# Optimization experiments

Measured on AMD Instinct MI355X. Metric: run time of the kernel, lower is better.

## Reference

```python
import jax, jax.numpy as jnp
import numpy as np

B, N, D, H, T = 2048, 128, 256, 8, 64
HD = D // H
TANH_C = 10.0
MASK_PENALTY = 1e9


def setup_inputs() -> dict:
    key = jax.random.key(0)
    ks = jax.random.split(key, 16)
    s = 1.0 / np.sqrt(D).astype(np.float32)
    w = lambda k: jax.random.normal(k, (D, D), jnp.float32) * s
    return {
        'node_emb': jax.random.normal(ks[0], (B, N, D), jnp.float32),
        'graph_emb': jax.random.normal(ks[1], (B, D), jnp.float32),
        'W_target': w(ks[2]), 'W_global': w(ks[3]),
        'W_K1': w(ks[4]), 'W_K2': w(ks[5]),
        'W_Q': w(ks[6]), 'W_V': w(ks[7]),
        'Wq_m': w(ks[8]), 'Wk_m': w(ks[9]), 'Wv_m': w(ks[10]), 'Wo_m': w(ks[11]),
        'targets': jax.random.randint(ks[12], (T, B), 0, N, jnp.int32),
        'masks': jax.random.randint(ks[13], (T, B, N), 0, 2, jnp.int32),
    }


def _mha(q, k, v, Wq, Wk, Wv, Wo):
    # q: [B,1,D]; k,v: [B,N,D]. Standard multi-head attention (glimpse).
    qh = (q @ Wq.T).reshape(B, 1, H, HD).transpose(0, 2, 1, 3)   # [B,H,1,HD]
    kh = (k @ Wk.T).reshape(B, N, H, HD).transpose(0, 2, 1, 3)   # [B,H,N,HD]
    vh = (v @ Wv.T).reshape(B, N, H, HD).transpose(0, 2, 1, 3)
    scores = jnp.einsum('bhqd,bhnd->bhqn', qh, kh) / np.sqrt(HD).astype(np.float32)
    attn = jax.nn.softmax(scores, axis=-1)
    out = jnp.einsum('bhqn,bhnd->bhqd', attn, vh)                # [B,H,1,HD]
    out = out.transpose(0, 2, 1, 3).reshape(B, 1, D)
    return out @ Wo.T


def reference(node_emb, graph_emb, W_target, W_global, W_K1, W_K2, W_Q, W_V,
              Wq_m, Wk_m, Wv_m, Wo_m, targets, masks):
    # Step-invariant projections (embeddings fixed across decode steps here).
    keys = node_emb @ W_K1.T      # [B,N,D]
    vals = node_emb @ W_V.T       # [B,N,D]
    key2 = node_emb @ W_K2.T      # [B,N,D]
    g_ctx = graph_emb @ W_global.T  # [B,D]
    inv_sqrt_d = np.float32(1.0 / np.sqrt(D))

    def step(ll, tm):
        tgt, mask = tm  # tgt:[B] int32, mask:[B,N] int32
        tgt_emb = jnp.take_along_axis(node_emb, tgt[:, None, None], axis=1)[:, 0, :]  # [B,D]
        context = (tgt_emb @ W_target.T + g_ctx)[:, None, :]      # [B,1,D]
        glimpse = _mha(context, keys, vals, Wq_m, Wk_m, Wv_m, Wo_m)  # [B,1,D]
        query = glimpse @ W_Q.T                                    # [B,1,D]
        logits = jnp.einsum('bqd,bnd->bn', query, key2) * inv_sqrt_d  # [B,N]
        logits = TANH_C * jnp.tanh(logits) - mask.astype(jnp.float32) * MASK_PENALTY
        log_p = jax.nn.log_softmax(logits, axis=1)
        actions = jnp.argmax(log_p, axis=1)                        # greedy TopKSampler
        ll = ll + jnp.take_along_axis(log_p, actions[:, None], axis=1)[:, 0]
        return ll, None

    ll, _ = jax.lax.scan(step, jnp.zeros(B, jnp.float32), (targets, masks))
    return ll
```

## Files before the change

kernel.cpp:

```cpp
#include <hip/hip_runtime.h>
#include <hip/hip_bf16.h>

#define BB 2048
#define NN 128
#define DD 256
#define HH 8
#define TT 64

typedef __bf16 bf16x8 __attribute__((ext_vector_type(8)));
typedef float f32x4 __attribute__((ext_vector_type(4)));

static __device__ __forceinline__ f32x4 mfma16(bf16x8 a, bf16x8 b, f32x4 c) {
  return __builtin_amdgcn_mfma_f32_16x16x32_bf16(a, b, c, 0, 0, 0);
}

static __device__ __forceinline__ f32x4 zero4() {
  f32x4 z = {0.f, 0.f, 0.f, 0.f};
  return z;
}

static __device__ __forceinline__ bf16x8 cvt8(const float* p) {
  const float4 x0 = *(const float4*)p;
  const float4 x1 = *(const float4*)(p + 4);
  bf16x8 r;
  r[0] = (__bf16)x0.x; r[1] = (__bf16)x0.y; r[2] = (__bf16)x0.z; r[3] = (__bf16)x0.w;
  r[4] = (__bf16)x1.x; r[5] = (__bf16)x1.y; r[6] = (__bf16)x1.z; r[7] = (__bf16)x1.w;
  return r;
}

static __device__ __forceinline__ unsigned pk2(float a, float b) {
  __bf16 x = (__bf16)a, y = (__bf16)b;
  unsigned short ux, uy;
  __builtin_memcpy(&ux, &x, 2);
  __builtin_memcpy(&uy, &y, 2);
  return (unsigned)ux | ((unsigned)uy << 16);
}

static __device__ __forceinline__ float fast_tanh10(float y) {
  const float e = __expf(2.f * y);
  return 10.f - 20.f * __builtin_amdgcn_rcpf(1.f + e);
}

__global__ void fold1(const float* __restrict__ Wq_m, const float* __restrict__ W_target,
                      const float* __restrict__ W_global, const float* __restrict__ Wk_m,
                      const float* __restrict__ W_K1, const float* __restrict__ Wv_m,
                      const float* __restrict__ W_V, const float* __restrict__ W_Q,
                      const float* __restrict__ Wo_m,
                      __bf16* __restrict__ WTQ, float* __restrict__ WGQT,
                      __bf16* __restrict__ WKH, __bf16* __restrict__ WVH,
                      float* __restrict__ WQO) {
  const int p = blockIdx.x >> 8;
  const int i = blockIdx.x & 255;
  const int t = threadIdx.x;
  __shared__ float arow[256];
  const float* A;
  const float* Bm;
  if (p == 0)      { A = Wq_m; Bm = W_target; }
  else if (p == 1) { A = Wq_m; Bm = W_global; }
  else if (p == 2) { A = Wk_m; Bm = W_K1; }
  else if (p == 3) { A = Wv_m; Bm = W_V; }
  else             { A = W_Q;  Bm = Wo_m; }
  arow[t] = A[i * 256 + t];
  __syncthreads();
  float acc = 0.f;
  for (int k = 0; k < 256; ++k) acc = fmaf(arow[k], Bm[k * 256 + t], acc);
  if (p == 0)      WTQ[i * 256 + t] = (__bf16)acc;
  else if (p == 1) WGQT[t * 256 + i] = acc;
  else if (p == 2) WKH[i * 256 + t] = (__bf16)acc;
  else if (p == 3) WVH[i * 256 + t] = (__bf16)acc;
  else             WQO[i * 256 + t] = acc;
}

__global__ void fold2(const float* __restrict__ WQO, const float* __restrict__ W_K2,
                      __bf16* __restrict__ WZL) {
  const int j = blockIdx.x;
  const int t = threadIdx.x;
  __shared__ float col[256];
  col[t] = W_K2[t * 256 + j];
  __syncthreads();
  float acc = 0.f;
  for (int d = 0; d < 256; ++d) acc = fmaf(WQO[d * 256 + t], col[d], acc);
  WZL[j * 256 + t] = (__bf16)acc;
}

__global__ void gq_kernel(const float* __restrict__ ge, const float* __restrict__ WGQT,
                          float* __restrict__ GQ) {
  const int b0 = blockIdx.x * 8;
  const int t = threadIdx.x;
  __shared__ float g[8][256];
#pragma unroll
  for (int i = 0; i < 8; ++i) g[i][t] = ge[(b0 + i) * 256 + t];
  __syncthreads();
  float acc[8] = {0.f, 0.f, 0.f, 0.f, 0.f, 0.f, 0.f, 0.f};
  for (int j = 0; j < 256; ++j) {
    const float wv = WGQT[j * 256 + t];
#pragma unroll
    for (int i = 0; i < 8; ++i) acc[i] = fmaf(wv, g[i][j], acc[i]);
  }
#pragma unroll
  for (int i = 0; i < 8; ++i) GQ[(b0 + i) * 256 + t] = acc[i];
}

__global__ __launch_bounds__(512)
void kvq_kernel(const float* __restrict__ E, const int* __restrict__ tg,
                const __bf16* __restrict__ WKH, const __bf16* __restrict__ WVH,
                const __bf16* __restrict__ WTQ, const float* __restrict__ GQ,
                __bf16* __restrict__ KH, __bf16* __restrict__ VT,
                __bf16* __restrict__ Qb, __bf16* __restrict__ Ebf) {
  const int b = blockIdx.x;
  const int tid = threadIdx.x;
  const int w = tid >> 6;
  const int l = tid & 63;
  const int lr = l & 15;
  const int lg = l >> 4;
  __shared__ __align__(16) __bf16 Es[128 * 264];
  __shared__ int tgs[64];
  if (tid < 64) tgs[tid] = tg[tid * BB + b];
  const float* Eb = E + (size_t)b * NN * DD;
  __bf16* Ebfb = Ebf + (size_t)b * NN * DD;
#pragma unroll
  for (int it = 0; it < 8; ++it) {
    const int c = it * 512 + tid;
    const int row = c >> 5;
    const int c8 = c & 31;
    const bf16x8 v = cvt8(Eb + row * 256 + c8 * 8);
    *(bf16x8*)&Es[row * 264 + c8 * 8] = v;
    *(bf16x8*)(Ebfb + row * 256 + c8 * 8) = v;
  }
  __syncthreads();

  {
    f32x4 akk[8][2];
    f32x4 avv[2][8];
#pragma unroll
    for (int mf = 0; mf < 8; ++mf)
#pragma unroll
      for (int nf = 0; nf < 2; ++nf) akk[mf][nf] = zero4();
#pragma unroll
    for (int mf = 0; mf < 2; ++mf)
#pragma unroll
      for (int nf = 0; nf < 8; ++nf) avv[mf][nf] = zero4();

    for (int kk = 0; kk < 8; ++kk) {
      bf16x8 e[8], wk[2], wv[2];
#pragma unroll
      for (int i = 0; i < 8; ++i)
        e[i] = *(const bf16x8*)&Es[(i * 16 + lr) * 264 + kk * 32 + lg * 8];
#pragma unroll
      for (int nf = 0; nf < 2; ++nf) {
        const size_t wo = (size_t)(w * 32 + nf * 16 + lr) * DD + kk * 32 + lg * 8;
        wk[nf] = *(const bf16x8*)(WKH + wo);
        wv[nf] = *(const bf16x8*)(WVH + wo);
      }
#pragma unroll
      for (int mf = 0; mf < 8; ++mf)
#pragma unroll
        for (int nf = 0; nf < 2; ++nf) akk[mf][nf] = mfma16(e[mf], wk[nf], akk[mf][nf]);
#pragma unroll
      for (int mf = 0; mf < 2; ++mf)
#pragma unroll
        for (int nf = 0; nf < 8; ++nf) avv[mf][nf] = mfma16(wv[mf], e[nf], avv[mf][nf]);
    }

    __bf16* KHb = KH + (size_t)b * NN * DD;
#pragma unroll
    for (int mf = 0; mf < 8; ++mf)
#pragma unroll
      for (int nf = 0; nf < 2; ++nf)
#pragma unroll
        for (int r = 0; r < 4; ++r)
          KHb[(mf * 16 + lg * 4 + r) * DD + w * 32 + nf * 16 + lr] = (__bf16)akk[mf][nf][r];

    __bf16* VTb = VT + (size_t)b * DD * NN;
#pragma unroll
    for (int mf = 0; mf < 2; ++mf)
#pragma unroll
      for (int nf = 0; nf < 8; ++nf)
#pragma unroll
        for (int r = 0; r < 4; ++r)
          VTb[(w * 32 + mf * 16 + lg * 4 + r) * NN + nf * 16 + lr] = (__bf16)avv[mf][nf][r];
  }

  {
    f32x4 acc[4][2];
#pragma unroll
    for (int mf = 0; mf < 4; ++mf)
#pragma unroll
      for (int nf = 0; nf < 2; ++nf) acc[mf][nf] = zero4();
    int rowoff[4];
#pragma unroll
    for (int mf = 0; mf < 4; ++mf) rowoff[mf] = tgs[mf * 16 + lr] * 264;
    for (int kk = 0; kk < 8; ++kk) {
      bf16x8 aF[4], bF[2];
#pragma unroll
      for (int mf = 0; mf < 4; ++mf)
        aF[mf] = *(const bf16x8*)&Es[rowoff[mf] + kk * 32 + lg * 8];
#pragma unroll
      for (int nf = 0; nf < 2; ++nf)
        bF[nf] = *(const bf16x8*)(WTQ + (size_t)(w * 32 + nf * 16 + lr) * DD + kk * 32 + lg * 8);
#pragma unroll
      for (int mf = 0; mf < 4; ++mf)
#pragma unroll
        for (int nf = 0; nf < 2; ++nf) acc[mf][nf] = mfma16(aF[mf], bF[nf], acc[mf][nf]);
    }
#pragma unroll
    for (int nf = 0; nf < 2; ++nf) {
      const int col = w * 32 + nf * 16 + lr;
      const float g = GQ[b * DD + col];
#pragma unroll
      for (int mf = 0; mf < 4; ++mf)
#pragma unroll
        for (int r = 0; r < 4; ++r)
          Qb[((size_t)b * TT + mf * 16 + lg * 4 + r) * DD + col] = (__bf16)(acc[mf][nf][r] + g);
    }
  }
}

__global__ __launch_bounds__(256)
void attn4_kernel(const __bf16* __restrict__ Qb, const __bf16* __restrict__ KH,
                  const __bf16* __restrict__ VT, __bf16* __restrict__ HO) {
  const int j = (blockIdx.x & 7) * ((BB * 4) / 8) + (blockIdx.x >> 3);
  const int b = j >> 2;
  const int c0 = (j & 3) * 64;
  const int tid = threadIdx.x;
  const int w = tid >> 6;
  const int l = tid & 63;
  const int lr = l & 15;
  const int lg = l >> 4;
  const int T0 = w * 16;

  __shared__ __align__(16) __bf16 KHs[128 * 72];
  __shared__ __align__(16) __bf16 VTs[64 * 136];
  __shared__ __align__(16) __bf16 Ps[4][16 * 136];

  const __bf16* KHb = KH + (size_t)b * NN * DD;
  const __bf16* VTb = VT + (size_t)b * DD * NN;

  bf16x8 aq[2];
#pragma unroll
  for (int h = 0; h < 2; ++h)
    aq[h] = *(const bf16x8*)(Qb + ((size_t)b * TT + T0 + lr) * DD + c0 + h * 32 + lg * 8);

#pragma unroll
  for (int it = 0; it < 4; ++it) {
    const int c = it * 256 + tid;
    const int row = c >> 3;
    const int c8 = c & 7;
    *(bf16x8*)&KHs[row * 72 + c8 * 8] = *(const bf16x8*)(KHb + (size_t)row * DD + c0 + c8 * 8);
  }
#pragma unroll
  for (int it = 0; it < 4; ++it) {
    const int c = it * 256 + tid;
    const int row = c >> 4;
    const int c8 = c & 15;
    *(bf16x8*)&VTs[row * 136 + c8 * 8] =
        *(const bf16x8*)(VTb + (size_t)(c0 + row) * NN + c8 * 8);
  }
  __syncthreads();

  __bf16* myp = Ps[w];
  __bf16* HOb = HO + (size_t)b * TT * DD + c0;

#pragma unroll
  for (int h = 0; h < 2; ++h) {
    f32x4 s[8];
#pragma unroll
    for (int nf = 0; nf < 8; ++nf)
      s[nf] = mfma16(*(const bf16x8*)&KHs[(nf * 16 + lr) * 72 + h * 32 + lg * 8], aq[h], zero4());

    float mx = -1e30f;
#pragma unroll
    for (int nf = 0; nf < 8; ++nf)
#pragma unroll
      for (int r = 0; r < 4; ++r) mx = fmaxf(mx, s[nf][r]);
    mx = fmaxf(mx, __shfl_xor(mx, 16));
    mx = fmaxf(mx, __shfl_xor(mx, 32));

    float sm = 0.f;
    uint2 evp[8];
#pragma unroll
    for (int nf = 0; nf < 8; ++nf) {
      const float e0 = __expf((s[nf][0] - mx) * 0.17677669529663687f);
      const float e1 = __expf((s[nf][1] - mx) * 0.17677669529663687f);
      const float e2 = __expf((s[nf][2] - mx) * 0.17677669529663687f);
      const float e3 = __expf((s[nf][3] - mx) * 0.17677669529663687f);
      sm += (e0 + e1) + (e2 + e3);
      evp[nf].x = pk2(e0, e1);
      evp[nf].y = pk2(e2, e3);
    }
    sm += __shfl_xor(sm, 16);
    sm += __shfl_xor(sm, 32);

#pragma unroll
    for (int nf = 0; nf < 8; ++nf)
      *(uint2*)&myp[lr * 136 + nf * 16 + lg * 4] = evp[nf];

    f32x4 o0 = zero4(), o1 = zero4();
#pragma unroll
    for (int kk = 0; kk < 4; ++kk) {
      const bf16x8 ap = *(const bf16x8*)&myp[lr * 136 + kk * 32 + lg * 8];
      o0 = mfma16(ap, *(const bf16x8*)&VTs[(h * 32 + lr) * 136 + kk * 32 + lg * 8], o0);
      o1 = mfma16(ap, *(const bf16x8*)&VTs[(h * 32 + 16 + lr) * 136 + kk * 32 + lg * 8], o1);
    }
#pragma unroll
    for (int r = 0; r < 4; ++r) {
      const float inv = __builtin_amdgcn_rcpf(__shfl(sm, lg * 4 + r));
      HOb[(size_t)(T0 + lg * 4 + r) * DD + h * 32 + lr] = (__bf16)(o0[r] * inv);
      HOb[(size_t)(T0 + lg * 4 + r) * DD + h * 32 + 16 + lr] = (__bf16)(o1[r] * inv);
    }
  }
}

__global__ __launch_bounds__(256)
void zlog2_kernel(const __bf16* __restrict__ Ebf, const __bf16* __restrict__ HO,
                  const __bf16* __restrict__ WZL, const int* __restrict__ MK,
                  float* __restrict__ out) {
  const int b = blockIdx.x;
  const int tid = threadIdx.x;
  const int w = tid >> 6;
  const int l = tid & 63;
  const int lr = l & 15;
  const int lg = l >> 4;
  const int T0 = w * 16;
  __shared__ __align__(16) __bf16 Zs[64 * 264];
  __shared__ float red[4];

  const __bf16* Eb = Ebf + (size_t)b * NN * DD;
  const __bf16* HOb = HO + (size_t)b * TT * DD;

  {
    f32x4 acc[4][4];
#pragma unroll
    for (int mf = 0; mf < 4; ++mf)
#pragma unroll
      for (int nf = 0; nf < 4; ++nf) acc[mf][nf] = zero4();
    for (int kk = 0; kk < 8; ++kk) {
      bf16x8 aF[4], bF[4];
#pragma unroll
      for (int mf = 0; mf < 4; ++mf)
        aF[mf] = *(const bf16x8*)(HOb + (size_t)(mf * 16 + lr) * DD + kk * 32 + lg * 8);
#pragma unroll
      for (int nf = 0; nf < 4; ++nf)
        bF[nf] = *(const bf16x8*)(WZL + (size_t)(w * 64 + nf * 16 + lr) * DD + kk * 32 + lg * 8);
#pragma unroll
      for (int mf = 0; mf < 4; ++mf)
#pragma unroll
        for (int nf = 0; nf < 4; ++nf) acc[mf][nf] = mfma16(aF[mf], bF[nf], acc[mf][nf]);
    }
#pragma unroll
    for (int mf = 0; mf < 4; ++mf)
#pragma unroll
      for (int nf = 0; nf < 4; ++nf)
#pragma unroll
        for (int r = 0; r < 4; ++r)
          Zs[(mf * 16 + lg * 4 + r) * 264 + w * 64 + nf * 16 + lr] = (__bf16)acc[mf][nf][r];
  }
  __syncthreads();

  {
    f32x4 sa[8];
#pragma unroll
    for (int nf = 0; nf < 8; ++nf) sa[nf] = zero4();
    for (int kk = 0; kk < 8; ++kk) {
      const bf16x8 bZ = *(const bf16x8*)&Zs[(T0 + lr) * 264 + kk * 32 + lg * 8];
#pragma unroll
      for (int nf = 0; nf < 8; ++nf) {
        const bf16x8 aE = *(const bf16x8*)(Eb + (size_t)(nf * 16 + lr) * DD + kk * 32 + lg * 8);
        sa[nf] = mfma16(aE, bZ, sa[nf]);
      }
    }
    const int t = T0 + lr;
    float xs[8][4];
    float mx = -3e38f;
#pragma unroll
    for (int nf = 0; nf < 8; ++nf) {
      const int4 mk4 = *(const int4*)(MK + ((size_t)t * BB + b) * NN + nf * 16 + lg * 4);
      xs[nf][0] = fast_tanh10(sa[nf][0] * 0.0625f) - (float)mk4.x * 1e9f;
      xs[nf][1] = fast_tanh10(sa[nf][1] * 0.0625f) - (float)mk4.y * 1e9f;
      xs[nf][2] = fast_tanh10(sa[nf][2] * 0.0625f) - (float)mk4.z * 1e9f;
      xs[nf][3] = fast_tanh10(sa[nf][3] * 0.0625f) - (float)mk4.w * 1e9f;
      mx = fmaxf(mx, fmaxf(fmaxf(xs[nf][0], xs[nf][1]), fmaxf(xs[nf][2], xs[nf][3])));
    }
    mx = fmaxf(mx, __shfl_xor(mx, 16));
    mx = fmaxf(mx, __shfl_xor(mx, 32));
    float sm = 0.f;
#pragma unroll
    for (int nf = 0; nf < 8; ++nf)
#pragma unroll
      for (int r = 0; r < 4; ++r) sm += __expf(xs[nf][r] - mx);
    sm += __shfl_xor(sm, 16);
    sm += __shfl_xor(sm, 32);
    float part = logf(sm);
    part += __shfl_xor(part, 1);
    part += __shfl_xor(part, 2);
    part += __shfl_xor(part, 4);
    part += __shfl_xor(part, 8);
    if (l == 0) red[w] = part;
  }
  __syncthreads();
  if (tid == 0) out[b] = -(red[0] + red[1] + red[2] + red[3]);
}

extern "C" void kernel_launch(void* const* d_in, const int* in_sizes, int n_in,
                              void* d_out, int out_size, void* d_ws, size_t ws_size,
                              hipStream_t stream) {
  (void)in_sizes; (void)n_in; (void)out_size; (void)ws_size;
  const float* node_emb  = (const float*)d_in[0];
  const float* graph_emb = (const float*)d_in[1];
  const float* W_target  = (const float*)d_in[2];
  const float* W_global  = (const float*)d_in[3];
  const float* W_K1      = (const float*)d_in[4];
  const float* W_K2      = (const float*)d_in[5];
  const float* W_Q       = (const float*)d_in[6];
  const float* W_V       = (const float*)d_in[7];
  const float* Wq_m      = (const float*)d_in[8];
  const float* Wk_m      = (const float*)d_in[9];
  const float* Wv_m      = (const float*)d_in[10];
  const float* Wo_m      = (const float*)d_in[11];
  const int* targets     = (const int*)d_in[12];
  const int* masks       = (const int*)d_in[13];

  char* p = (char*)d_ws;
  __bf16* Ebf = (__bf16*)p; p += (size_t)BB * NN * DD * 2;
  __bf16* KH  = (__bf16*)p; p += (size_t)BB * NN * DD * 2;
  __bf16* VT  = (__bf16*)p; p += (size_t)BB * DD * NN * 2;
  __bf16* HO  = (__bf16*)p; p += (size_t)BB * TT * DD * 2;
  __bf16* Qb  = (__bf16*)p; p += (size_t)BB * TT * DD * 2;
  __bf16* WTQ = (__bf16*)p; p += 256 * 256 * 2;
  __bf16* WKH = (__bf16*)p; p += 256 * 256 * 2;
  __bf16* WVH = (__bf16*)p; p += 256 * 256 * 2;
  __bf16* WZL = (__bf16*)p; p += 256 * 256 * 2;
  float* WGQT = (float*)p;  p += 256 * 256 * 4;
  float* WQO  = (float*)p;  p += 256 * 256 * 4;
  float* GQ   = (float*)p;  p += (size_t)BB * DD * 4;

  fold1<<<1280, 256, 0, stream>>>(Wq_m, W_target, W_global, Wk_m, W_K1, Wv_m, W_V, W_Q, Wo_m,
                                  WTQ, WGQT, WKH, WVH, WQO);
  fold2<<<256, 256, 0, stream>>>(WQO, W_K2, WZL);
  gq_kernel<<<BB / 8, 256, 0, stream>>>(graph_emb, WGQT, GQ);
  kvq_kernel<<<BB, 512, 0, stream>>>(node_emb, targets, WKH, WVH, WTQ, GQ, KH, VT, Qb, Ebf);
  attn4_kernel<<<BB * 4, 256, 0, stream>>>(Qb, KH, VT, HO);
  zlog2_kernel<<<BB, 256, 0, stream>>>(Ebf, HO, WZL, masks, (float*)d_out);
}
```

Measured before the change: 500.6 us.

## Move query projection from kv kernel into attention kernel, drop Qb buffer

The per-target query projection (gathered node embedding times WTQ plus the graph term) is no longer computed in the KV projection kernel and written to a global Qb buffer. Each attention block now computes only its 64-column slice of the query for its 16 targets with MFMA, reading the bf16 embedding row and WTQ directly. The result is staged through the per-warp shared scratch and loaded as fragments. This removes the Qb write and read round trip and lightens the KV kernel. In exchange, each of the four column-blocks per batch re-gathers embedding rows and reads a WTQ slice from global memory.

```diff
diff --git a/kernel.cpp b/kernel.cpp
--- a/kernel.cpp
+++ b/kernel.cpp
@@ -102,11 +102,9 @@
 }
 
 __global__ __launch_bounds__(512)
-void kvq_kernel(const float* __restrict__ E, const int* __restrict__ tg,
-                const __bf16* __restrict__ WKH, const __bf16* __restrict__ WVH,
-                const __bf16* __restrict__ WTQ, const float* __restrict__ GQ,
-                __bf16* __restrict__ KH, __bf16* __restrict__ VT,
-                __bf16* __restrict__ Qb, __bf16* __restrict__ Ebf) {
+void kv_kernel(const float* __restrict__ E, const __bf16* __restrict__ WKH,
+               const __bf16* __restrict__ WVH, __bf16* __restrict__ KH,
+               __bf16* __restrict__ VT, __bf16* __restrict__ Ebf) {
   const int b = blockIdx.x;
   const int tid = threadIdx.x;
   const int w = tid >> 6;
@@ -114,8 +112,6 @@
   const int lr = l & 15;
   const int lg = l >> 4;
   __shared__ __align__(16) __bf16 Es[128 * 264];
-  __shared__ int tgs[64];
-  if (tid < 64) tgs[tid] = tg[tid * BB + b];
   const float* Eb = E + (size_t)b * NN * DD;
   __bf16* Ebfb = Ebf + (size_t)b * NN * DD;
 #pragma unroll
@@ -129,96 +125,62 @@
   }
   __syncthreads();
 
-  {
-    f32x4 akk[8][2];
-    f32x4 avv[2][8];
+  f32x4 akk[8][2];
+  f32x4 avv[2][8];
+#pragma unroll
+  for (int mf = 0; mf < 8; ++mf)
+#pragma unroll
+    for (int nf = 0; nf < 2; ++nf) akk[mf][nf] = zero4();
+#pragma unroll
+  for (int mf = 0; mf < 2; ++mf)
+#pragma unroll
+    for (int nf = 0; nf < 8; ++nf) avv[mf][nf] = zero4();
+
+  for (int kk = 0; kk < 8; ++kk) {
+    bf16x8 e[8], wk[2], wv[2];
+#pragma unroll
+    for (int i = 0; i < 8; ++i)
+      e[i] = *(const bf16x8*)&Es[(i * 16 + lr) * 264 + kk * 32 + lg * 8];
+#pragma unroll
+    for (int nf = 0; nf < 2; ++nf) {
+      const size_t wo = (size_t)(w * 32 + nf * 16 + lr) * DD + kk * 32 + lg * 8;
+      wk[nf] = *(const bf16x8*)(WKH + wo);
+      wv[nf] = *(const bf16x8*)(WVH + wo);
+    }
 #pragma unroll
     for (int mf = 0; mf < 8; ++mf)
 #pragma unroll
-      for (int nf = 0; nf < 2; ++nf) akk[mf][nf] = zero4();
+      for (int nf = 0; nf < 2; ++nf) akk[mf][nf] = mfma16(e[mf], wk[nf], akk[mf][nf]);
 #pragma unroll
     for (int mf = 0; mf < 2; ++mf)
 #pragma unroll
-      for (int nf = 0; nf < 8; ++nf) avv[mf][nf] = zero4();
-
-    for (int kk = 0; kk < 8; ++kk) {
-      bf16x8 e[8], wk[2], wv[2];
-#pragma unroll
-      for (int i = 0; i < 8; ++i)
-        e[i] = *(const bf16x8*)&Es[(i * 16 + lr) * 264 + kk * 32 + lg * 8];
-#pragma unroll
-      for (int nf = 0; nf < 2; ++nf) {
-        const size_t wo = (size_t)(w * 32 + nf * 16 + lr) * DD + kk * 32 + lg * 8;
-        wk[nf] = *(const bf16x8*)(WKH + wo);
-        wv[nf] = *(const bf16x8*)(WVH + wo);
-      }
-#pragma unroll
-      for (int mf = 0; mf < 8; ++mf)
-#pragma unroll
-        for (int nf = 0; nf < 2; ++nf) akk[mf][nf] = mfma16(e[mf], wk[nf], akk[mf][nf]);
-#pragma unroll
-      for (int mf = 0; mf < 2; ++mf)
-#pragma unroll
-        for (int nf = 0; nf < 8; ++nf) avv[mf][nf] = mfma16(wv[mf], e[nf], avv[mf][nf]);
-    }
-
-    __bf16* KHb = KH + (size_t)b * NN * DD;
-#pragma unroll
-    for (int mf = 0; mf < 8; ++mf)
-#pragma unroll
-      for (int nf = 0; nf < 2; ++nf)
-#pragma unroll
-        for (int r = 0; r < 4; ++r)
-          KHb[(mf * 16 + lg * 4 + r) * DD + w * 32 + nf * 16 + lr] = (__bf16)akk[mf][nf][r];
-
-    __bf16* VTb = VT + (size_t)b * DD * NN;
-#pragma unroll
-    for (int mf = 0; mf < 2; ++mf)
-#pragma unroll
-      for (int nf = 0; nf < 8; ++nf)
-#pragma unroll
-        for (int r = 0; r < 4; ++r)
-          VTb[(w * 32 + mf * 16 + lg * 4 + r) * NN + nf * 16 + lr] = (__bf16)avv[mf][nf][r];
-  }
-
-  {
-    f32x4 acc[4][2];
-#pragma unroll
-    for (int mf = 0; mf < 4; ++mf)
-#pragma unroll
-      for (int nf = 0; nf < 2; ++nf) acc[mf][nf] = zero4();
-    int rowoff[4];
-#pragma unroll
-    for (int mf = 0; mf < 4; ++mf) rowoff[mf] = tgs[mf * 16 + lr] * 264;
-    for (int kk = 0; kk < 8; ++kk) {
-      bf16x8 aF[4], bF[2];
-#pragma unroll
-      for (int mf = 0; mf < 4; ++mf)
-        aF[mf] = *(const bf16x8*)&Es[rowoff[mf] + kk * 32 + lg * 8];
-#pragma unroll
-      for (int nf = 0; nf < 2; ++nf)
-        bF[nf] = *(const bf16x8*)(WTQ + (size_t)(w * 32 + nf * 16 + lr) * DD + kk * 32 + lg * 8);
-#pragma unroll
-      for (int mf = 0; mf < 4; ++mf)
-#pragma unroll
-        for (int nf = 0; nf < 2; ++nf) acc[mf][nf] = mfma16(aF[mf], bF[nf], acc[mf][nf]);
-    }
-#pragma unroll
-    for (int nf = 0; nf < 2; ++nf) {
-      const int col = w * 32 + nf * 16 + lr;
-      const float g = GQ[b * DD + col];
-#pragma unroll
-      for (int mf = 0; mf < 4; ++mf)
-#pragma unroll
-        for (int r = 0; r < 4; ++r)
-          Qb[((size_t)b * TT + mf * 16 + lg * 4 + r) * DD + col] = (__bf16)(acc[mf][nf][r] + g);
-    }
-  }
+      for (int nf = 0; nf < 8; ++nf) avv[mf][nf] = mfma16(wv[mf], e[nf], avv[mf][nf]);
+  }
+
+  __bf16* KHb = KH + (size_t)b * NN * DD;
+#pragma unroll
+  for (int mf = 0; mf < 8; ++mf)
+#pragma unroll
+    for (int nf = 0; nf < 2; ++nf)
+#pragma unroll
+      for (int r = 0; r < 4; ++r)
+        KHb[(mf * 16 + lg * 4 + r) * DD + w * 32 + nf * 16 + lr] = (__bf16)akk[mf][nf][r];
+
+  __bf16* VTb = VT + (size_t)b * DD * NN;
+#pragma unroll
+  for (int mf = 0; mf < 2; ++mf)
+#pragma unroll
+    for (int nf = 0; nf < 8; ++nf)
+#pragma unroll
+      for (int r = 0; r < 4; ++r)
+        VTb[(w * 32 + mf * 16 + lg * 4 + r) * NN + nf * 16 + lr] = (__bf16)avv[mf][nf][r];
 }
 
 __global__ __launch_bounds__(256)
-void attn4_kernel(const __bf16* __restrict__ Qb, const __bf16* __restrict__ KH,
-                  const __bf16* __restrict__ VT, __bf16* __restrict__ HO) {
+void attn5_kernel(const __bf16* __restrict__ Ebf, const int* __restrict__ tg,
+                  const __bf16* __restrict__ WTQ, const float* __restrict__ GQ,
+                  const __bf16* __restrict__ KH, const __bf16* __restrict__ VT,
+                  __bf16* __restrict__ HO) {
   const int j = (blockIdx.x & 7) * ((BB * 4) / 8) + (blockIdx.x >> 3);
   const int b = j >> 2;
   const int c0 = (j & 3) * 64;
@@ -233,13 +195,12 @@
   __shared__ __align__(16) __bf16 VTs[64 * 136];
   __shared__ __align__(16) __bf16 Ps[4][16 * 136];
 
+  const __bf16* Eb = Ebf + (size_t)b * NN * DD;
   const __bf16* KHb = KH + (size_t)b * NN * DD;
   const __bf16* VTb = VT + (size_t)b * DD * NN;
-
-  bf16x8 aq[2];
-#pragma unroll
-  for (int h = 0; h < 2; ++h)
-    aq[h] = *(const bf16x8*)(Qb + ((size_t)b * TT + T0 + lr) * DD + c0 + h * 32 + lg * 8);
+  __bf16* myp = Ps[w];
+
+  const int node = tg[(T0 + lr) * BB + b];
 
 #pragma unroll
   for (int it = 0; it < 4; ++it) {
@@ -256,9 +217,31 @@
     *(bf16x8*)&VTs[row * 136 + c8 * 8] =
         *(const bf16x8*)(VTb + (size_t)(c0 + row) * NN + c8 * 8);
   }
-  __syncthreads();
-
-  __bf16* myp = Ps[w];
+
+  {
+    f32x4 qa[4] = {zero4(), zero4(), zero4(), zero4()};
+    for (int kk = 0; kk < 8; ++kk) {
+      const bf16x8 aF = *(const bf16x8*)(Eb + (size_t)node * DD + kk * 32 + lg * 8);
+#pragma unroll
+      for (int nf = 0; nf < 4; ++nf) {
+        const bf16x8 bF =
+            *(const bf16x8*)(WTQ + (size_t)(c0 + nf * 16 + lr) * DD + kk * 32 + lg * 8);
+        qa[nf] = mfma16(aF, bF, qa[nf]);
+      }
+    }
+#pragma unroll
+    for (int nf = 0; nf < 4; ++nf) {
+      const float g = GQ[b * DD + c0 + nf * 16 + lr];
+#pragma unroll
+      for (int r = 0; r < 4; ++r)
+        myp[(lg * 4 + r) * 72 + nf * 16 + lr] = (__bf16)(qa[nf][r] + g);
+    }
+  }
+  bf16x8 aq[2];
+#pragma unroll
+  for (int h = 0; h < 2; ++h) aq[h] = *(const bf16x8*)&myp[lr * 72 + h * 32 + lg * 8];
+  __syncthreads();
+
   __bf16* HOb = HO + (size_t)b * TT * DD + c0;
 
 #pragma unroll
@@ -425,7 +408,6 @@
   __bf16* KH  = (__bf16*)p; p += (size_t)BB * NN * DD * 2;
   __bf16* VT  = (__bf16*)p; p += (size_t)BB * DD * NN * 2;
   __bf16* HO  = (__bf16*)p; p += (size_t)BB * TT * DD * 2;
-  __bf16* Qb  = (__bf16*)p; p += (size_t)BB * TT * DD * 2;
   __bf16* WTQ = (__bf16*)p; p += 256 * 256 * 2;
   __bf16* WKH = (__bf16*)p; p += 256 * 256 * 2;
   __bf16* WVH = (__bf16*)p; p += 256 * 256 * 2;
@@ -438,7 +420,7 @@
                                   WTQ, WGQT, WKH, WVH, WQO);
   fold2<<<256, 256, 0, stream>>>(WQO, W_K2, WZL);
   gq_kernel<<<BB / 8, 256, 0, stream>>>(graph_emb, WGQT, GQ);
-  kvq_kernel<<<BB, 512, 0, stream>>>(node_emb, targets, WKH, WVH, WTQ, GQ, KH, VT, Qb, Ebf);
-  attn4_kernel<<<BB * 4, 256, 0, stream>>>(Qb, KH, VT, HO);
+  kv_kernel<<<BB, 512, 0, stream>>>(node_emb, WKH, WVH, KH, VT, Ebf);
+  attn5_kernel<<<BB * 4, 256, 0, stream>>>(Ebf, targets, WTQ, GQ, KH, VT, HO);
   zlog2_kernel<<<BB, 256, 0, stream>>>(Ebf, HO, WZL, masks, (float*)d_out);
 }
```

New measurement: 595.4 us. 1.19x slower.
